# Kernel optimization log

Hardware: AMD Instinct MI355X
Metric: run time of the kernel (lower is better)

The kernel has to match this reference:

```python
import jax, jax.numpy as jnp
import numpy as np

N_HEADS = 16
ROPE_THETA = 10000.0


def _rotate_half(x):
    d = x.shape[-1] // 2
    return jnp.concatenate([-x[..., d:], x[..., :d]], axis=-1)


def setup_inputs() -> dict:
    key = jax.random.key(0)
    k1, k2, k3, k4 = jax.random.split(key, 4)
    B, S, D = 2, 2048, 2048
    std = 0.02
    return {
        "x": jax.random.normal(k1, (B, S, D), dtype=jnp.float32),
        "wq": std * jax.random.normal(k2, (D, D), dtype=jnp.float32),
        "wkv": std * jax.random.normal(k3, (D, 2 * D), dtype=jnp.float32),
        "wo": std * jax.random.normal(k4, (D, D), dtype=jnp.float32),
    }


def reference(x, wq, wkv, wo):
    # prefill case: kv_cache=None, past_length=0
    B, S, D = x.shape
    H = N_HEADS
    dh = D // H

    Q = x @ wq.T                                   # [B,S,D]
    K, V = jnp.split(x @ wkv, 2, axis=-1)          # [B,S,D] each

    q = Q.reshape(B, S, H, dh).transpose(0, 2, 1, 3)  # [B,H,S,dh]
    k = K.reshape(B, S, H, dh).transpose(0, 2, 1, 3)
    v = V.reshape(B, S, H, dh).transpose(0, 2, 1, 3)

    # RoPE tables (cos/sin of outer(pos, inv_freq), duplicated across halves)
    inv_freq = 1.0 / (ROPE_THETA ** (jnp.arange(0, dh, 2, dtype=jnp.float32) / dh))
    emb = jnp.arange(S, dtype=jnp.float32)[:, None] * inv_freq[None, :]  # [S, dh/2]
    cos = jnp.tile(jnp.cos(emb), (1, 2))[None, None]  # [1,1,S,dh]
    sin = jnp.tile(jnp.sin(emb), (1, 2))[None, None]

    q = q * cos + _rotate_half(q) * sin
    k = k * cos + _rotate_half(k) * sin

    scale = 1.0 / jnp.sqrt(jnp.asarray(dh, dtype=x.dtype))
    scores = jnp.einsum('bhqd,bhkd->bhqk', q, k) * scale  # [B,H,S,S]
    causal = jnp.tril(jnp.ones((S, S), dtype=bool))
    scores = jnp.where(causal[None, None], scores, -jnp.inf)
    attn = jax.nn.softmax(scores, axis=-1)

    out = jnp.einsum('bhqk,bhkd->bhqd', attn, v)          # [B,H,S,dh]
    out = out.transpose(0, 2, 1, 3).reshape(B, S, D)
    return out @ wo.T
```

## Files before the change

### kernel.cpp

```cpp
#include <hip/hip_runtime.h>
#include <stdint.h>

typedef unsigned short u16;
typedef __attribute__((ext_vector_type(8))) short short8;
typedef __attribute__((ext_vector_type(4))) float floatx4;

#define MFMA16(a, b, c) __builtin_amdgcn_mfma_f32_16x16x32_bf16(a, b, c, 0, 0, 0)

static __device__ __forceinline__ void gl_lds16(const void* g, void* l) {
  __builtin_amdgcn_global_load_lds(
      (const __attribute__((address_space(1))) uint32_t*)g,
      (__attribute__((address_space(3))) uint32_t*)l, 16, 0, 0);
}

static __device__ __forceinline__ float b2f(u16 u) {
  union { float f; unsigned u; } v;
  v.u = ((unsigned)u) << 16;
  return v.f;
}
static __device__ __forceinline__ u16 f2b(float f) {
  union { float f; unsigned u; } v;
  v.f = f;
  unsigned r = v.u + 0x7fffu + ((v.u >> 16) & 1u);
  return (u16)(r >> 16);
}

template <int CTRL>
static __device__ __forceinline__ float dppf(float x) {
  return __builtin_bit_cast(
      float, __builtin_amdgcn_update_dpp(0, __builtin_bit_cast(int, x), CTRL,
                                         0xF, 0xF, true));
}
static __device__ __forceinline__ float sum16(float x) {
  x += dppf<0x128>(x);
  x += dppf<0x124>(x);
  x += dppf<0x122>(x);
  x += dppf<0x121>(x);
  return x;
}
static __device__ __forceinline__ float max16(float x) {
  x = fmaxf(x, dppf<0x128>(x));
  x = fmaxf(x, dppf<0x124>(x));
  x = fmaxf(x, dppf<0x122>(x));
  x = fmaxf(x, dppf<0x121>(x));
  return x;
}

__global__ __launch_bounds__(256) void detect_f32(const u16* __restrict__ x,
                                                  int* __restrict__ flag) {
  __shared__ int cnt[256];
  int c = 0;
  for (int i = threadIdx.x; i < 65536; i += 256) {
    int e = (x[i] >> 7) & 0xFF;
    if (e >= 140) ++c;
  }
  cnt[threadIdx.x] = c;
  __syncthreads();
  for (int s = 128; s > 0; s >>= 1) {
    if (threadIdx.x < (unsigned)s) cnt[threadIdx.x] += cnt[threadIdx.x + s];
    __syncthreads();
  }
  if (threadIdx.x == 0) *flag = (cnt[0] > 1000) ? 1 : 0;
}

__global__ __launch_bounds__(256) void convert_in8(const void* __restrict__ src,
                                                   u16* __restrict__ dst, int n8,
                                                   const int* __restrict__ flag) {
  int i = blockIdx.x * 256 + threadIdx.x;
  if (i >= n8) return;
  short8 r;
  if (*flag) {
    const float4* s = (const float4*)src;
    float4 a = s[2 * i], b = s[2 * i + 1];
    r[0] = (short)f2b(a.x); r[1] = (short)f2b(a.y);
    r[2] = (short)f2b(a.z); r[3] = (short)f2b(a.w);
    r[4] = (short)f2b(b.x); r[5] = (short)f2b(b.y);
    r[6] = (short)f2b(b.z); r[7] = (short)f2b(b.w);
  } else {
    r = ((const short8*)src)[i];
  }
  ((short8*)dst)[i] = r;
}

__global__ __launch_bounds__(256) void transpose_conv(const void* __restrict__ in,
                                                      u16* __restrict__ out,
                                                      int R, int Ccols,
                                                      const int* __restrict__ flag) {
  __shared__ u16 tile[32][33];
  int f = *flag;
  int c0 = blockIdx.x * 32, r0 = blockIdx.y * 32;
  int lx = threadIdx.x & 31, ly = threadIdx.x >> 5;
#pragma unroll
  for (int i = 0; i < 32; i += 8) {
    size_t idx = (size_t)(r0 + ly + i) * Ccols + c0 + lx;
    tile[ly + i][lx] = f ? f2b(((const float*)in)[idx]) : ((const u16*)in)[idx];
  }
  __syncthreads();
#pragma unroll
  for (int i = 0; i < 32; i += 8)
    out[(size_t)(c0 + ly + i) * R + r0 + lx] = tile[lx][ly + i];
}

__global__ __launch_bounds__(256) void transpose_v(const u16* __restrict__ KV,
                                                   u16* __restrict__ Vt) {
  __shared__ u16 tile[32][33];
  int b = blockIdx.z;
  int d0 = blockIdx.x * 32, s0 = blockIdx.y * 32;
  int lx = threadIdx.x & 31, ly = threadIdx.x >> 5;
  const u16* src = KV + ((size_t)(b * 2048 + s0)) * 4096 + 2048 + d0;
#pragma unroll
  for (int i = 0; i < 32; i += 8)
    tile[ly + i][lx] = src[(size_t)(ly + i) * 4096 + lx];
  __syncthreads();
  u16* dst = Vt + ((size_t)(b * 2048 + d0)) * 2048 + s0;
#pragma unroll
  for (int i = 0; i < 32; i += 8)
    dst[(size_t)(ly + i) * 2048 + lx] = tile[lx][ly + i];
}

__global__ __launch_bounds__(256) void gemm_nt(const u16* __restrict__ A,
                                               const u16* __restrict__ Bm,
                                               void* __restrict__ Cv,
                                               int M, int N, int K,
                                               const int* __restrict__ flag,
                                               int flag_mode) {
  __shared__ u16 Ash[128 * 64];
  __shared__ u16 Bsh[128 * 64];
  int tid = threadIdx.x, w = tid >> 6, lane = tid & 63;
  int quad = lane >> 4, l15 = lane & 15;
  int m0 = blockIdx.y * 128, n0 = blockIdx.x * 128;
  int wm = (w & 1) * 64, wn = (w >> 1) * 64;
  int f32out = flag_mode ? *flag : 0;

  floatx4 acc[4][4];
#pragma unroll
  for (int i = 0; i < 4; ++i)
#pragma unroll
    for (int j = 0; j < 4; ++j) acc[i][j] = floatx4{0.f, 0.f, 0.f, 0.f};

  int srow = lane >> 3;
  int gch = (lane & 7) ^ srow;
  const u16* Ag = A + (size_t)(m0 + w * 32 + srow) * K + gch * 8;
  const u16* Bg = Bm + (size_t)(n0 + w * 32 + srow) * K + gch * 8;

  for (int k0 = 0; k0 < K; k0 += 64) {
    __syncthreads();
#pragma unroll
    for (int t = 0; t < 4; ++t) {
      gl_lds16(Ag + (size_t)t * 8 * K + k0, (void*)(Ash + (w * 32 + t * 8) * 64));
      gl_lds16(Bg + (size_t)t * 8 * K + k0, (void*)(Bsh + (w * 32 + t * 8) * 64));
    }
    __syncthreads();
#pragma unroll
    for (int kk = 0; kk < 2; ++kk) {
      int c = kk * 4 + quad;
      short8 af[4], bf[4];
#pragma unroll
      for (int i = 0; i < 4; ++i) {
        int m = wm + 16 * i + l15;
        af[i] = *(const short8*)(Ash + m * 64 + ((c ^ (m & 7)) << 3));
        int n = wn + 16 * i + l15;
        bf[i] = *(const short8*)(Bsh + n * 64 + ((c ^ (n & 7)) << 3));
      }
#pragma unroll
      for (int i = 0; i < 4; ++i)
#pragma unroll
        for (int j = 0; j < 4; ++j) acc[i][j] = MFMA16(af[i], bf[j], acc[i][j]);
    }
  }

#pragma unroll
  for (int i = 0; i < 4; ++i)
#pragma unroll
    for (int r = 0; r < 4; ++r) {
      int row = m0 + wm + 16 * i + quad * 4 + r;
      if (f32out) {
        float* cp = (float*)Cv + (size_t)row * N + n0 + wn + l15;
#pragma unroll
        for (int j = 0; j < 4; ++j) cp[16 * j] = acc[i][j][r];
      } else {
        u16* cp = (u16*)Cv + (size_t)row * N + n0 + wn + l15;
#pragma unroll
        for (int j = 0; j < 4; ++j) cp[16 * j] = f2b(acc[i][j][r]);
      }
    }
}

__global__ __launch_bounds__(512, 2) void gemm8(const u16* __restrict__ A,
                                                const u16* __restrict__ Bm,
                                                void* __restrict__ Cv,
                                                int M, int N, int K,
                                                const int* __restrict__ flag,
                                                int flag_mode) {
  __shared__ u16 Ash[2 * 256 * 64];
  __shared__ u16 Bsh[2 * 256 * 64];
  int tid = threadIdx.x, w = tid >> 6, lane = tid & 63;
  int quad = lane >> 4, l15 = lane & 15;
  int wr = w >> 2, wc = w & 3;
  int wm = wr * 128, wn = wc * 64;
  int m0 = blockIdx.y * 256, n0 = blockIdx.x * 256;
  int f32out = flag_mode ? *flag : 0;
  const int NT = K >> 6;

  int srow8 = lane >> 3;
  int gch = (lane & 7) ^ srow8;
  const u16* Ag = A + (size_t)(m0 + w * 8 + srow8) * K + gch * 8;
  const u16* Bg = Bm + (size_t)(n0 + w * 8 + srow8) * K + gch * 8;
  int ldsrow = w * 8;

  floatx4 acc[8][4];
#pragma unroll
  for (int i = 0; i < 8; ++i)
#pragma unroll
    for (int j = 0; j < 4; ++j) acc[i][j] = floatx4{0.f, 0.f, 0.f, 0.f};

  int ch0 = ((quad ^ (l15 & 7)) << 3);
  int ch1 = (((4 + quad) ^ (l15 & 7)) << 3);

  auto stage = [&](int qi) {
    int tau = qi >> 2;
    int tc = tau < NT ? tau : NT - 1;
    int hh = qi & 3;
    int half = (hh & 1) * 128;
    int sbuf = (tau & 1) * (256 * 64);
    size_t kof = (size_t)tc * 64;
    if (hh < 2) {
      gl_lds16(Bg + (size_t)half * K + kof,
               (void*)(Bsh + sbuf + (half + ldsrow) * 64));
      gl_lds16(Bg + (size_t)(half + 64) * K + kof,
               (void*)(Bsh + sbuf + (half + 64 + ldsrow) * 64));
    } else {
      gl_lds16(Ag + (size_t)half * K + kof,
               (void*)(Ash + sbuf + (half + ldsrow) * 64));
      gl_lds16(Ag + (size_t)(half + 64) * K + kof,
               (void*)(Ash + sbuf + (half + 64 + ldsrow) * 64));
    }
  };

  stage(0); stage(1); stage(2); stage(3);
  __asm__ volatile("s_waitcnt vmcnt(4)" ::: "memory");
  stage(4); stage(5); stage(6);
  __asm__ volatile("s_waitcnt vmcnt(6)" ::: "memory");
  __builtin_amdgcn_s_barrier();

  for (int t = 0; t < NT; ++t) {
    u16* As = Ash + (t & 1) * (256 * 64);
    u16* Bs = Bsh + (t & 1) * (256 * 64);
    if (t) {
      __asm__ volatile("s_waitcnt vmcnt(6)" ::: "memory");
      __builtin_amdgcn_s_barrier();
    }
    int qb = 7 + 4 * t;
    short8 bf[8], af0[8], af1[8];

#pragma unroll
    for (int j = 0; j < 4; ++j) {
      int n = wn + 16 * j + l15;
      bf[2 * j] = *(const short8*)(Bs + n * 64 + ch0);
    }
#pragma unroll
    for (int i = 0; i < 4; ++i) {
      int m = wm + 16 * i + l15;
      af0[2 * i] = *(const short8*)(As + m * 64 + ch0);
    }
    stage(qb);
    __builtin_amdgcn_s_barrier();
    __asm__ volatile("s_waitcnt lgkmcnt(0)" ::: "memory");
    __builtin_amdgcn_sched_barrier(0);
    __builtin_amdgcn_s_setprio(1);
#pragma unroll
    for (int i = 0; i < 4; ++i)
#pragma unroll
      for (int j = 0; j < 4; ++j)
        acc[i][j] = MFMA16(af0[2 * i], bf[2 * j], acc[i][j]);
    __builtin_amdgcn_s_setprio(0);
    __builtin_amdgcn_s_barrier();

#pragma unroll
    for (int j = 0; j < 4; ++j) {
      int n = wn + 16 * j + l15;
      bf[2 * j + 1] = *(const short8*)(Bs + n * 64 + ch1);
    }
#pragma unroll
    for (int i = 0; i < 4; ++i) {
      int m = wm + 16 * i + l15;
      af0[2 * i + 1] = *(const short8*)(As + m * 64 + ch1);
    }
    stage(qb + 1);
    __builtin_amdgcn_s_barrier();
    __asm__ volatile("s_waitcnt lgkmcnt(0)" ::: "memory");
    __builtin_amdgcn_sched_barrier(0);
    __builtin_amdgcn_s_setprio(1);
#pragma unroll
    for (int i = 0; i < 4; ++i)
#pragma unroll
      for (int j = 0; j < 4; ++j)
        acc[i][j] = MFMA16(af0[2 * i + 1], bf[2 * j + 1], acc[i][j]);
    __builtin_amdgcn_s_setprio(0);
    __builtin_amdgcn_s_barrier();

#pragma unroll
    for (int i = 0; i < 4; ++i) {
      int m = wm + 64 + 16 * i + l15;
      af1[2 * i] = *(const short8*)(As + m * 64 + ch0);
    }
    stage(qb + 2);
    __builtin_amdgcn_s_barrier();
    __asm__ volatile("s_waitcnt lgkmcnt(0)" ::: "memory");
    __builtin_amdgcn_sched_barrier(0);
    __builtin_amdgcn_s_setprio(1);
#pragma unroll
    for (int i = 0; i < 4; ++i)
#pragma unroll
      for (int j = 0; j < 4; ++j)
        acc[4 + i][j] = MFMA16(af1[2 * i], bf[2 * j], acc[4 + i][j]);
    __builtin_amdgcn_s_setprio(0);
    __builtin_amdgcn_s_barrier();

#pragma unroll
    for (int i = 0; i < 4; ++i) {
      int m = wm + 64 + 16 * i + l15;
      af1[2 * i + 1] = *(const short8*)(As + m * 64 + ch1);
    }
    stage(qb + 3);
    __builtin_amdgcn_s_barrier();
    __asm__ volatile("s_waitcnt lgkmcnt(0)" ::: "memory");
    __builtin_amdgcn_sched_barrier(0);
    __builtin_amdgcn_s_setprio(1);
#pragma unroll
    for (int i = 0; i < 4; ++i)
#pragma unroll
      for (int j = 0; j < 4; ++j)
        acc[4 + i][j] = MFMA16(af1[2 * i + 1], bf[2 * j + 1], acc[4 + i][j]);
    __builtin_amdgcn_s_setprio(0);
    __builtin_amdgcn_s_barrier();
  }

#pragma unroll
  for (int i = 0; i < 8; ++i)
#pragma unroll
    for (int r = 0; r < 4; ++r) {
      int row = m0 + wm + 16 * i + quad * 4 + r;
      if (f32out) {
        float* cp = (float*)Cv + (size_t)row * N + n0 + wn + l15;
#pragma unroll
        for (int j = 0; j < 4; ++j) cp[16 * j] = acc[i][j][r];
      } else {
        u16* cp = (u16*)Cv + (size_t)row * N + n0 + wn + l15;
#pragma unroll
        for (int j = 0; j < 4; ++j) cp[16 * j] = f2b(acc[i][j][r]);
      }
    }
}

__global__ __launch_bounds__(256) void rope_kernel(u16* __restrict__ Q,
                                                   u16* __restrict__ KV) {
  const float scale = 0.08838834764831845f;
  int idx = blockIdx.x * 256 + threadIdx.x;
  int tok = idx >> 10;
  int rem = idx & 1023;
  int h = rem >> 6, i = rem & 63;
  int pos = tok & 2047;
  float f = __powf(10000.0f, -(float)(2 * i) * (1.0f / 128.0f));
  float ang = (float)pos * f;
  float s, c;
  sincosf(ang, &s, &c);

  size_t qb = (size_t)tok * 2048 + h * 128 + i;
  float q1 = b2f(Q[qb]), q2 = b2f(Q[qb + 64]);
  Q[qb] = f2b((q1 * c - q2 * s) * scale);
  Q[qb + 64] = f2b((q2 * c + q1 * s) * scale);

  size_t kb = (size_t)tok * 4096 + h * 128 + i;
  float k1 = b2f(KV[kb]), k2 = b2f(KV[kb + 64]);
  KV[kb] = f2b(k1 * c - k2 * s);
  KV[kb + 64] = f2b(k2 * c + k1 * s);
}

__global__ __launch_bounds__(512, 1) void flash_attn(const u16* __restrict__ Q,
                                                     const u16* __restrict__ KV,
                                                     const u16* __restrict__ Vt,
                                                     u16* __restrict__ O) {
  const int S = 2048, D = 2048, KVld = 4096;
  int bh = blockIdx.x;
  int qt = 15 - (int)blockIdx.y;
  int b = bh >> 4, h = bh & 15;
  int tid = threadIdx.x, w = tid >> 6, lane = tid & 63;
  int quad = lane >> 4, l15 = lane & 15;

  const u16* Qb = Q + (size_t)(b * S) * D + h * 128;
  const u16* Kb = KV + (size_t)(b * S) * KVld + h * 128;
  const u16* Vtb = Vt + ((size_t)(b * 2048 + h * 128)) * S;

  __shared__ u16 Ksh[2][64 * 128];
  __shared__ u16 Vsh[2][128 * 64];
  __shared__ u16 Psh[8][16 * 64];

  auto stage_kv = [&](int kt, int buf) {
    int kb = kt * 64;
#pragma unroll
    for (int tt = 0; tt < 2; ++tt) {
      int r0 = w * 8 + tt * 4;
      int row = r0 + quad;
      int g = (l15 & 8) | ((l15 & 7) ^ (row & 7));
      gl_lds16(Kb + (size_t)(kb + row) * KVld + g * 8,
               (void*)(Ksh[buf] + r0 * 128));
    }
#pragma unroll
    for (int tt = 0; tt < 2; ++tt) {
      int d0 = w * 16 + tt * 8;
      int d = d0 + (lane >> 3);
      int g = (lane & 7) ^ (d & 7);
      gl_lds16(Vtb + (size_t)d * S + kb + g * 8, (void*)(Vsh[buf] + d0 * 64));
    }
  };

  int qw = qt * 128 + w * 16;

  short8 qf[4];
  {
    const u16* qp = Qb + (size_t)(qw + l15) * D + quad * 8;
#pragma unroll
    for (int kk = 0; kk < 4; ++kk) qf[kk] = *(const short8*)(qp + kk * 32);
  }

  floatx4 o[8];
#pragma unroll
  for (int t = 0; t < 8; ++t) o[t] = floatx4{0.f, 0.f, 0.f, 0.f};
  float mrow[4], lrow[4];
#pragma unroll
  for (int r = 0; r < 4; ++r) { mrow[r] = -1e30f; lrow[r] = 0.f; }

  int nk = 2 * qt + 2;
  stage_kv(0, 0);
  __syncthreads();

  for (int kt = 0; kt < nk; ++kt) {
    int kb = kt * 64;
    int cur = kt & 1;
    if (kt + 1 < nk) stage_kv(kt + 1, cur ^ 1);

    if (kb <= qw + 15) {
      const u16* Kc = Ksh[cur];
      const u16* Vc = Vsh[cur];
      floatx4 sc[4];
#pragma unroll
      for (int nf = 0; nf < 4; ++nf) sc[nf] = floatx4{0.f, 0.f, 0.f, 0.f};
#pragma unroll
      for (int kk = 0; kk < 4; ++kk) {
        int c = kk * 4 + quad;
        short8 kf[4];
#pragma unroll
        for (int nf = 0; nf < 4; ++nf) {
          int n = nf * 16 + l15;
          int pc = (c & 8) | ((c & 7) ^ (n & 7));
          kf[nf] = *(const short8*)(Kc + n * 128 + pc * 8);
        }
#pragma unroll
        for (int nf = 0; nf < 4; ++nf) sc[nf] = MFMA16(qf[kk], kf[nf], sc[nf]);
      }

      bool masked = (kb + 63 > qw);
      floatx4 alv;
#pragma unroll
      for (int r = 0; r < 4; ++r) {
        int qg = qw + quad * 4 + r;
        float v0 = sc[0][r], v1 = sc[1][r];
        float v2 = sc[2][r], v3 = sc[3][r];
        if (masked) {
          v0 = (kb + l15 <= qg) ? v0 : -1e30f;
          v1 = (kb + 16 + l15 <= qg) ? v1 : -1e30f;
          v2 = (kb + 32 + l15 <= qg) ? v2 : -1e30f;
          v3 = (kb + 48 + l15 <= qg) ? v3 : -1e30f;
        }
        float mx = max16(fmaxf(fmaxf(v0, v1), fmaxf(v2, v3)));
        float mn = fmaxf(mrow[r], mx);
        float al = __expf(mrow[r] - mn);
        mrow[r] = mn;
        float p0 = __expf(v0 - mn), p1 = __expf(v1 - mn);
        float p2 = __expf(v2 - mn), p3 = __expf(v3 - mn);
        float rs = sum16((p0 + p1) + (p2 + p3));
        lrow[r] = lrow[r] * al + rs;
        alv[r] = al;
        int m_ = quad * 4 + r;
        int sw = (m_ & 3) ^ ((m_ >> 2) << 1);
        int cb = l15 >> 3, e = l15 & 7;
        u16* pr = Psh[w] + m_ * 64;
        pr[(((0 + cb) ^ sw) << 3) + e] = f2b(p0);
        pr[(((2 + cb) ^ sw) << 3) + e] = f2b(p1);
        pr[(((4 + cb) ^ sw) << 3) + e] = f2b(p2);
        pr[(((6 + cb) ^ sw) << 3) + e] = f2b(p3);
      }
#pragma unroll
      for (int t = 0; t < 8; ++t) o[t] *= alv;
      __asm__ volatile("s_waitcnt lgkmcnt(0)" ::: "memory");

#pragma unroll
      for (int ks = 0; ks < 2; ++ks) {
        int c = ks * 4 + quad;
        int psw = (l15 & 3) ^ ((l15 >> 2) << 1);
        short8 pf = *(const short8*)(Psh[w] + l15 * 64 + ((c ^ psw) << 3));
#pragma unroll
        for (int t = 0; t < 8; ++t) {
          int d = t * 16 + l15;
          short8 vf = *(const short8*)(Vc + d * 64 + ((c ^ (d & 7)) << 3));
          o[t] = MFMA16(pf, vf, o[t]);
        }
      }
    }
    __syncthreads();
  }

#pragma unroll
  for (int r = 0; r < 4; ++r) {
    float inv = 1.0f / lrow[r];
    int qg = qw + quad * 4 + r;
    u16* op = O + (size_t)(b * S + qg) * D + h * 128;
#pragma unroll
    for (int t = 0; t < 8; ++t) op[t * 16 + l15] = f2b(o[t][r] * inv);
  }
}

extern "C" void kernel_launch(void* const* d_in, const int* in_sizes, int n_in,
                              void* d_out, int out_size, void* d_ws, size_t ws_size,
                              hipStream_t stream) {
  const void* x = d_in[0];
  const void* wq = d_in[1];
  const void* wkv = d_in[2];
  const void* wo = d_in[3];

  int* flag = (int*)d_ws;
  u16* xb = (u16*)d_ws + 64;
  u16* Wbuf = xb + (size_t)8388608;
  u16* Qb = Wbuf + (size_t)8388608;
  u16* KVb = Qb + (size_t)8388608;
  u16* AO = xb;

  detect_f32<<<1, 256, 0, stream>>>((const u16*)x, flag);
  convert_in8<<<4096, 256, 0, stream>>>(x, xb, 1048576, flag);
  convert_in8<<<2048, 256, 0, stream>>>(wq, Wbuf, 524288, flag);
  gemm_nt<<<dim3(16, 32), 256, 0, stream>>>(xb, Wbuf, Qb, 4096, 2048, 2048, flag, 0);
  transpose_conv<<<dim3(128, 64), 256, 0, stream>>>(wkv, Wbuf, 2048, 4096, flag);
  gemm8<<<dim3(16, 16), 512, 0, stream>>>(xb, Wbuf, KVb, 4096, 4096, 2048, flag, 0);
  transpose_v<<<dim3(64, 64, 2), 256, 0, stream>>>(KVb, Wbuf);
  rope_kernel<<<16384, 256, 0, stream>>>(Qb, KVb);
  flash_attn<<<dim3(32, 16), 512, 0, stream>>>(Qb, KVb, Wbuf, AO);
  convert_in8<<<2048, 256, 0, stream>>>(wo, Wbuf, 524288, flag);
  gemm_nt<<<dim3(16, 32), 256, 0, stream>>>(AO, Wbuf, d_out, 4096, 2048, 2048, flag, 1);
}
```

Before: 478.6 us.

## Single-buffer K in flash attention, parallelize dtype detection, skip redundant rescale

Flash attention now keeps one K buffer in LDS. The next K/V tile is prefetched after a barrier that follows the QK^T MFMAs, and V stays double-buffered. The output rescale is skipped when every lane's alpha equals one, and P is rounded to bf16 with a cheaper round-to-nearest. The dtype detection kernel now runs across 32 blocks with vector loads and an atomic count, with a memset and a threshold moved into each consumer. These changes cut LDS use and serial detection latency, in exchange for an extra barrier per tile and slightly different rounding.

```diff
diff --git a/kernel.cpp b/kernel.cpp
--- a/kernel.cpp
+++ b/kernel.cpp
@@ -23,6 +23,11 @@
   v.f = f;
   unsigned r = v.u + 0x7fffu + ((v.u >> 16) & 1u);
   return (u16)(r >> 16);
+}
+static __device__ __forceinline__ u16 f2b_rn(float f) {
+  union { float f; unsigned u; } v;
+  v.f = f;
+  return (u16)((v.u + 0x8000u) >> 16);
 }
 
 template <int CTRL>
@@ -49,10 +54,13 @@
 __global__ __launch_bounds__(256) void detect_f32(const u16* __restrict__ x,
                                                   int* __restrict__ flag) {
   __shared__ int cnt[256];
+  int i = blockIdx.x * 256 + threadIdx.x;
+  short8 v = ((const short8*)x)[i];
   int c = 0;
-  for (int i = threadIdx.x; i < 65536; i += 256) {
-    int e = (x[i] >> 7) & 0xFF;
-    if (e >= 140) ++c;
+#pragma unroll
+  for (int j = 0; j < 8; ++j) {
+    int e = (((unsigned short)v[j]) >> 7) & 0xFF;
+    c += (e >= 140) ? 1 : 0;
   }
   cnt[threadIdx.x] = c;
   __syncthreads();
@@ -60,7 +68,7 @@
     if (threadIdx.x < (unsigned)s) cnt[threadIdx.x] += cnt[threadIdx.x + s];
     __syncthreads();
   }
-  if (threadIdx.x == 0) *flag = (cnt[0] > 1000) ? 1 : 0;
+  if (threadIdx.x == 0) atomicAdd(flag, cnt[0]);
 }
 
 __global__ __launch_bounds__(256) void convert_in8(const void* __restrict__ src,
@@ -69,7 +77,7 @@
   int i = blockIdx.x * 256 + threadIdx.x;
   if (i >= n8) return;
   short8 r;
-  if (*flag) {
+  if (*flag > 1000) {
     const float4* s = (const float4*)src;
     float4 a = s[2 * i], b = s[2 * i + 1];
     r[0] = (short)f2b(a.x); r[1] = (short)f2b(a.y);
@@ -87,7 +95,7 @@
                                                       int R, int Ccols,
                                                       const int* __restrict__ flag) {
   __shared__ u16 tile[32][33];
-  int f = *flag;
+  int f = (*flag > 1000) ? 1 : 0;
   int c0 = blockIdx.x * 32, r0 = blockIdx.y * 32;
   int lx = threadIdx.x & 31, ly = threadIdx.x >> 5;
 #pragma unroll
@@ -130,7 +138,7 @@
   int quad = lane >> 4, l15 = lane & 15;
   int m0 = blockIdx.y * 128, n0 = blockIdx.x * 128;
   int wm = (w & 1) * 64, wn = (w >> 1) * 64;
-  int f32out = flag_mode ? *flag : 0;
+  int f32out = flag_mode ? (*flag > 1000) : 0;
 
   floatx4 acc[4][4];
 #pragma unroll
@@ -199,7 +207,7 @@
   int wr = w >> 2, wc = w & 3;
   int wm = wr * 128, wn = wc * 64;
   int m0 = blockIdx.y * 256, n0 = blockIdx.x * 256;
-  int f32out = flag_mode ? *flag : 0;
+  int f32out = flag_mode ? (*flag > 1000) : 0;
   const int NT = K >> 6;
 
   int srow8 = lane >> 3;
@@ -392,20 +400,22 @@
   const u16* Kb = KV + (size_t)(b * S) * KVld + h * 128;
   const u16* Vtb = Vt + ((size_t)(b * 2048 + h * 128)) * S;
 
-  __shared__ u16 Ksh[2][64 * 128];
+  __shared__ u16 Ksh[64 * 128];
   __shared__ u16 Vsh[2][128 * 64];
   __shared__ u16 Psh[8][16 * 64];
 
-  auto stage_kv = [&](int kt, int buf) {
+  auto stage_k = [&](int kt) {
     int kb = kt * 64;
 #pragma unroll
     for (int tt = 0; tt < 2; ++tt) {
       int r0 = w * 8 + tt * 4;
       int row = r0 + quad;
       int g = (l15 & 8) | ((l15 & 7) ^ (row & 7));
-      gl_lds16(Kb + (size_t)(kb + row) * KVld + g * 8,
-               (void*)(Ksh[buf] + r0 * 128));
-    }
+      gl_lds16(Kb + (size_t)(kb + row) * KVld + g * 8, (void*)(Ksh + r0 * 128));
+    }
+  };
+  auto stage_v = [&](int kt, int buf) {
+    int kb = kt * 64;
 #pragma unroll
     for (int tt = 0; tt < 2; ++tt) {
       int d0 = w * 16 + tt * 8;
@@ -432,18 +442,17 @@
   for (int r = 0; r < 4; ++r) { mrow[r] = -1e30f; lrow[r] = 0.f; }
 
   int nk = 2 * qt + 2;
-  stage_kv(0, 0);
+  stage_k(0);
+  stage_v(0, 0);
   __syncthreads();
 
   for (int kt = 0; kt < nk; ++kt) {
     int kb = kt * 64;
     int cur = kt & 1;
-    if (kt + 1 < nk) stage_kv(kt + 1, cur ^ 1);
-
-    if (kb <= qw + 15) {
-      const u16* Kc = Ksh[cur];
-      const u16* Vc = Vsh[cur];
-      floatx4 sc[4];
+    bool act = (kb <= qw + 15);
+
+    floatx4 sc[4];
+    if (act) {
 #pragma unroll
       for (int nf = 0; nf < 4; ++nf) sc[nf] = floatx4{0.f, 0.f, 0.f, 0.f};
 #pragma unroll
@@ -454,12 +463,19 @@
         for (int nf = 0; nf < 4; ++nf) {
           int n = nf * 16 + l15;
           int pc = (c & 8) | ((c & 7) ^ (n & 7));
-          kf[nf] = *(const short8*)(Kc + n * 128 + pc * 8);
+          kf[nf] = *(const short8*)(Ksh + n * 128 + pc * 8);
         }
 #pragma unroll
         for (int nf = 0; nf < 4; ++nf) sc[nf] = MFMA16(qf[kk], kf[nf], sc[nf]);
       }
-
+    }
+    __syncthreads();
+    if (kt + 1 < nk) {
+      stage_k(kt + 1);
+      stage_v(kt + 1, cur ^ 1);
+    }
+
+    if (act) {
       bool masked = (kb + 63 > qw);
       floatx4 alv;
 #pragma unroll
@@ -486,13 +502,16 @@
         int sw = (m_ & 3) ^ ((m_ >> 2) << 1);
         int cb = l15 >> 3, e = l15 & 7;
         u16* pr = Psh[w] + m_ * 64;
-        pr[(((0 + cb) ^ sw) << 3) + e] = f2b(p0);
-        pr[(((2 + cb) ^ sw) << 3) + e] = f2b(p1);
-        pr[(((4 + cb) ^ sw) << 3) + e] = f2b(p2);
-        pr[(((6 + cb) ^ sw) << 3) + e] = f2b(p3);
-      }
-#pragma unroll
-      for (int t = 0; t < 8; ++t) o[t] *= alv;
+        pr[(((0 + cb) ^ sw) << 3) + e] = f2b_rn(p0);
+        pr[(((2 + cb) ^ sw) << 3) + e] = f2b_rn(p1);
+        pr[(((4 + cb) ^ sw) << 3) + e] = f2b_rn(p2);
+        pr[(((6 + cb) ^ sw) << 3) + e] = f2b_rn(p3);
+      }
+      if (__any((alv[0] != 1.f) || (alv[1] != 1.f) ||
+                (alv[2] != 1.f) || (alv[3] != 1.f))) {
+#pragma unroll
+        for (int t = 0; t < 8; ++t) o[t] *= alv;
+      }
       __asm__ volatile("s_waitcnt lgkmcnt(0)" ::: "memory");
 
 #pragma unroll
@@ -503,7 +522,7 @@
 #pragma unroll
         for (int t = 0; t < 8; ++t) {
           int d = t * 16 + l15;
-          short8 vf = *(const short8*)(Vc + d * 64 + ((c ^ (d & 7)) << 3));
+          short8 vf = *(const short8*)(Vsh[cur] + d * 64 + ((c ^ (d & 7)) << 3));
           o[t] = MFMA16(pf, vf, o[t]);
         }
       }
@@ -536,7 +555,8 @@
   u16* KVb = Qb + (size_t)8388608;
   u16* AO = xb;
 
-  detect_f32<<<1, 256, 0, stream>>>((const u16*)x, flag);
+  hipMemsetAsync(flag, 0, sizeof(int), stream);
+  detect_f32<<<32, 256, 0, stream>>>((const u16*)x, flag);
   convert_in8<<<4096, 256, 0, stream>>>(x, xb, 1048576, flag);
   convert_in8<<<2048, 256, 0, stream>>>(wq, Wbuf, 524288, flag);
   gemm_nt<<<dim3(16, 32), 256, 0, stream>>>(xb, Wbuf, Qb, 4096, 2048, 2048, flag, 0);
```

After: 418.7 us. 12.5% less time.
